# Optimization experiments

Measured on AMD Instinct MI355X. Metric: run time of the kernel, lower is better.

The kernel has to match this reference:

```python
import jax, jax.numpy as jnp
import numpy as np
from jax import lax

KSIZE = 3
SIGMA = 0.3 * ((KSIZE - 1) * 0.5 - 1) + 0.8  # cv2 auto-sigma for k=3 -> 0.8

def _gauss_kernel(k, sigma):
    ax = np.arange(k, dtype=np.float64) - (k - 1) / 2
    xx, yy = np.meshgrid(ax, ax, indexing='ij')
    ker = np.exp(-(xx ** 2 + yy ** 2) / (2.0 * sigma ** 2))
    ker /= ker.sum()
    return jnp.asarray(ker, jnp.float32)

SCHARR_X = jnp.array([[-3., 0., 3.], [-10., 0., 10.], [-3., 0., 3.]], jnp.float32)
SCHARR_Y = SCHARR_X.T  # cv2.Scharr(dy=1)

def _conv2d_reflect(img, ker):
    # img: [B,1,H,W]; cross-correlation (like cv2.filter2D) with BORDER_REFLECT_101
    p = ker.shape[0] // 2
    img = jnp.pad(img, ((0, 0), (0, 0), (p, p), (p, p)), mode='reflect')
    return lax.conv_general_dilated(img, ker[None, None], (1, 1), 'VALID')

def setup_inputs() -> dict:
    key = jax.random.key(0)
    x = jax.random.uniform(key, (8, 3, 1024, 1024), dtype=jnp.float32) * 255.0
    return {"x": x}

def reference(x):
    B, C, H, W = x.shape
    # cv2 RGB2GRAY weights
    rgb_w = jnp.array([0.299, 0.587, 0.114], dtype=x.dtype)
    gray = jnp.einsum('bchw,c->bhw', x, rgb_w)[:, None]  # [B,1,H,W]
    blurred = _conv2d_reflect(gray, _gauss_kernel(KSIZE, SIGMA))
    sx = _conv2d_reflect(blurred, SCHARR_X)
    sy = _conv2d_reflect(blurred, SCHARR_Y)
    mag = jnp.sqrt(sx * sx + sy * sy)  # L2_gradient=True
    # forward returns gradient magnitude replicated across channels
    return jnp.broadcast_to(mag, (B, C, H, W))
```

## Files before the change

### kernel.cpp

```cpp
#include <hip/hip_runtime.h>
#include <math.h>


#define IMG_H 1024
#define IMG_W 1024
#define TH 16
#define TW 128
#define GY (TH + 4)
#define GX (TW + 4)
#define BYR (TH + 2)
#define BXC (TW + 2)

#define GW0 0.52201125f
#define GW1 0.23899437f

__global__ __launch_bounds__(256)
void edge_kernel(const float* __restrict__ in, float* __restrict__ out, int B) {
    __shared__ float sg[GY][GX];
    __shared__ float sb[BYR][BXC];

    const int tid = threadIdx.x;
    const int x0 = blockIdx.x * TW;
    const int y0 = blockIdx.y * TH;
    const int b  = blockIdx.z;

    const size_t plane = (size_t)IMG_H * IMG_W;
    const float* pr = in + (size_t)b * 3 * plane;
    const float* pg = pr + plane;
    const float* pb = pg + plane;

    for (int i = tid; i < GY * GX; i += 256) {
        int gy = i / GX;
        int gx = i - gy * GX;
        int y = y0 - 2 + gy;
        int x = x0 - 2 + gx;
        y = (y < 0) ? -y : ((y >= IMG_H) ? (2 * IMG_H - 2 - y) : y);
        x = (x < 0) ? -x : ((x >= IMG_W) ? (2 * IMG_W - 2 - x) : x);
        int idx = y * IMG_W + x;
        sg[gy][gx] = 0.299f * pr[idx] + 0.587f * pg[idx] + 0.114f * pb[idx];
    }
    __syncthreads();

    for (int i = tid; i < BYR * BXC; i += 256) {
        int by = i / BXC;
        int bx = i - by * BXC;
        float h0 = GW1 * sg[by    ][bx] + GW0 * sg[by    ][bx + 1] + GW1 * sg[by    ][bx + 2];
        float h1 = GW1 * sg[by + 1][bx] + GW0 * sg[by + 1][bx + 1] + GW1 * sg[by + 1][bx + 2];
        float h2 = GW1 * sg[by + 2][bx] + GW0 * sg[by + 2][bx + 1] + GW1 * sg[by + 2][bx + 2];
        sb[by][bx] = GW1 * h0 + GW0 * h1 + GW1 * h2;
    }
    __syncthreads();

    const int tx  = tid & (TW - 1);
    const int ty0 = tid >> 7;
    float* po = out + (size_t)b * 3 * plane;
    for (int ty = ty0; ty < TH; ty += 2) {
        float a00 = sb[ty    ][tx], a01 = sb[ty    ][tx + 1], a02 = sb[ty    ][tx + 2];
        float a10 = sb[ty + 1][tx],                           a12 = sb[ty + 1][tx + 2];
        float a20 = sb[ty + 2][tx], a21 = sb[ty + 2][tx + 1], a22 = sb[ty + 2][tx + 2];
        float sx = 3.0f * (a02 - a00) + 10.0f * (a12 - a10) + 3.0f * (a22 - a20);
        float sy = 3.0f * (a20 - a00) + 10.0f * (a21 - a01) + 3.0f * (a22 - a02);
        float mag = sqrtf(sx * sx + sy * sy);
        size_t o = (size_t)(y0 + ty) * IMG_W + (x0 + tx);
        po[o]             = mag;
        po[o + plane]     = mag;
        po[o + 2 * plane] = mag;
    }
}

extern "C" void kernel_launch(void* const* d_in, const int* in_sizes, int n_in,
                              void* d_out, int out_size, void* d_ws, size_t ws_size,
                              hipStream_t stream) {
    const float* in = (const float*)d_in[0];
    float* out = (float*)d_out;
    const int B = in_sizes[0] / (3 * IMG_H * IMG_W);
    dim3 grid(IMG_W / TW, IMG_H / TH, B);
    edge_kernel<<<grid, dim3(256), 0, stream>>>(in, out, B);
}
```

Baseline: 185.5 us.

## Replace shared-memory tiles with register-resident separable 5x5 combined filter per wavefront

Folds the Gaussian blur and Scharr operators into separable 5-tap row filters (smooth and derivative) and applies them to gray values held in registers. A ring buffer keeps five rows per thread, neighbour columns come from wavefront shuffles, and only a small per-row halo is loaded. All loads and stores are now float4, and shared memory and block barriers are removed. In exchange the per-thread register count goes up, and the edge handling is more intricate because reflection and clamping have to be emulated at tile borders.

```diff
diff --git a/kernel.cpp b/kernel.cpp
--- a/kernel.cpp
+++ b/kernel.cpp
@@ -4,67 +4,104 @@
 
 #define IMG_H 1024
 #define IMG_W 1024
-#define TH 16
-#define TW 128
-#define GY (TH + 4)
-#define GX (TW + 4)
-#define BYR (TH + 2)
-#define BXC (TW + 2)
+#define SH 16
+#define SW 256
 
-#define GW0 0.52201125f
-#define GW1 0.23899437f
+#define W0 0.52201125f
+#define W1 0.23899437f
+#define AV0 0.71698311f
+#define AV1 3.95597745f
+#define AV2 6.65407872f
+
+__device__ __forceinline__ float4 gray4(float4 r, float4 g, float4 b) {
+    float4 o;
+    o.x = 0.299f * r.x + 0.587f * g.x + 0.114f * b.x;
+    o.y = 0.299f * r.y + 0.587f * g.y + 0.114f * b.y;
+    o.z = 0.299f * r.z + 0.587f * g.z + 0.114f * b.z;
+    o.w = 0.299f * r.w + 0.587f * g.w + 0.114f * b.w;
+    return o;
+}
 
 __global__ __launch_bounds__(256)
 void edge_kernel(const float* __restrict__ in, float* __restrict__ out, int B) {
-    __shared__ float sg[GY][GX];
-    __shared__ float sb[BYR][BXC];
+    const int tid  = threadIdx.x;
+    const int lane = tid & 63;
+    const int gw   = blockIdx.x * 4 + (tid >> 6);
 
-    const int tid = threadIdx.x;
-    const int x0 = blockIdx.x * TW;
-    const int y0 = blockIdx.y * TH;
-    const int b  = blockIdx.z;
+    const int ys = gw & 63;
+    const int xs = (gw >> 6) & 3;
+    const int b  = gw >> 8;
+
+    const int x0 = xs * SW;
+    const int y0 = ys * SH;
+    const int cb = x0 + 4 * lane;
 
     const size_t plane = (size_t)IMG_H * IMG_W;
     const float* pr = in + (size_t)b * 3 * plane;
     const float* pg = pr + plane;
     const float* pb = pg + plane;
+    float* po = out + (size_t)b * 3 * plane;
 
-    for (int i = tid; i < GY * GX; i += 256) {
-        int gy = i / GX;
-        int gx = i - gy * GX;
-        int y = y0 - 2 + gy;
-        int x = x0 - 2 + gx;
-        y = (y < 0) ? -y : ((y >= IMG_H) ? (2 * IMG_H - 2 - y) : y);
-        x = (x < 0) ? -x : ((x >= IMG_W) ? (2 * IMG_W - 2 - x) : x);
-        int idx = y * IMG_W + x;
-        sg[gy][gx] = 0.299f * pr[idx] + 0.587f * pg[idx] + 0.114f * pb[idx];
-    }
-    __syncthreads();
+    int hx = (lane == 0) ? (x0 - 4) : (x0 + SW);
+    hx = min(max(hx, 0), IMG_W - 4);
 
-    for (int i = tid; i < BYR * BXC; i += 256) {
-        int by = i / BXC;
-        int bx = i - by * BXC;
-        float h0 = GW1 * sg[by    ][bx] + GW0 * sg[by    ][bx + 1] + GW1 * sg[by    ][bx + 2];
-        float h1 = GW1 * sg[by + 1][bx] + GW0 * sg[by + 1][bx + 1] + GW1 * sg[by + 1][bx + 2];
-        float h2 = GW1 * sg[by + 2][bx] + GW0 * sg[by + 2][bx + 1] + GW1 * sg[by + 2][bx + 2];
-        sb[by][bx] = GW1 * h0 + GW0 * h1 + GW1 * h2;
-    }
-    __syncthreads();
+    float hs[5][4], hd[5][4];
 
-    const int tx  = tid & (TW - 1);
-    const int ty0 = tid >> 7;
-    float* po = out + (size_t)b * 3 * plane;
-    for (int ty = ty0; ty < TH; ty += 2) {
-        float a00 = sb[ty    ][tx], a01 = sb[ty    ][tx + 1], a02 = sb[ty    ][tx + 2];
-        float a10 = sb[ty + 1][tx],                           a12 = sb[ty + 1][tx + 2];
-        float a20 = sb[ty + 2][tx], a21 = sb[ty + 2][tx + 1], a22 = sb[ty + 2][tx + 2];
-        float sx = 3.0f * (a02 - a00) + 10.0f * (a12 - a10) + 3.0f * (a22 - a20);
-        float sy = 3.0f * (a20 - a00) + 10.0f * (a21 - a01) + 3.0f * (a22 - a02);
-        float mag = sqrtf(sx * sx + sy * sy);
-        size_t o = (size_t)(y0 + ty) * IMG_W + (x0 + tx);
-        po[o]             = mag;
-        po[o + plane]     = mag;
-        po[o + 2 * plane] = mag;
+    #pragma unroll
+    for (int t = 0; t < SH + 4; ++t) {
+        int yy = y0 - 2 + t;
+        yy = (yy < 0) ? -yy : ((yy >= IMG_H) ? (2 * IMG_H - 2 - yy) : yy);
+        const size_t ro = (size_t)yy << 10;
+
+        float4 r4 = *(const float4*)(pr + ro + cb);
+        float4 g4 = *(const float4*)(pg + ro + cb);
+        float4 b4 = *(const float4*)(pb + ro + cb);
+        float4 hr = *(const float4*)(pr + ro + hx);
+        float4 hg = *(const float4*)(pg + ro + hx);
+        float4 hb = *(const float4*)(pb + ro + hx);
+
+        float4 g   = gray4(r4, g4, b4);
+        float4 hgr = gray4(hr, hg, hb);
+
+        float lm2 = __shfl_up(g.z, 1);
+        float lm1 = __shfl_up(g.w, 1);
+        float rp1 = __shfl_down(g.x, 1);
+        float rp2 = __shfl_down(g.y, 1);
+        float rbx = __shfl(hgr.x, 1);
+        float rby = __shfl(hgr.y, 1);
+
+        lm2 = (lane == 0)  ? ((xs == 0) ? g.z : hgr.z) : lm2;
+        lm1 = (lane == 0)  ? ((xs == 0) ? g.y : hgr.w) : lm1;
+        rp1 = (lane == 63) ? ((xs == 3) ? g.z : rbx)   : rp1;
+        rp2 = (lane == 63) ? ((xs == 3) ? g.y : rby)   : rp2;
+
+        const float G[8] = {lm2, lm1, g.x, g.y, g.z, g.w, rp1, rp2};
+        const int ri = t % 5;
+        #pragma unroll
+        for (int k = 0; k < 4; ++k) {
+            hs[ri][k] = AV0 * (G[k] + G[k+4]) + AV1 * (G[k+1] + G[k+3]) + AV2 * G[k+2];
+            hd[ri][k] = W1 * (G[k+4] - G[k]) + W0 * (G[k+3] - G[k+1]);
+        }
+
+        if (t >= 4) {
+            const int i0 = (t+1) % 5, i1 = (t+2) % 5, i2 = (t+3) % 5,
+                      i3 = (t+4) % 5, i4 = t % 5;
+            float4 mag;
+            float* mp = &mag.x;
+            #pragma unroll
+            for (int k = 0; k < 4; ++k) {
+                float sx = AV0 * (hd[i0][k] + hd[i4][k])
+                         + AV1 * (hd[i1][k] + hd[i3][k])
+                         + AV2 * hd[i2][k];
+                float sy = W1 * (hs[i4][k] - hs[i0][k])
+                         + W0 * (hs[i3][k] - hs[i1][k]);
+                mp[k] = sqrtf(sx * sx + sy * sy);
+            }
+            size_t o = ((size_t)(y0 + t - 4) << 10) + cb;
+            *(float4*)(po + o)             = mag;
+            *(float4*)(po + o + plane)     = mag;
+            *(float4*)(po + o + 2 * plane) = mag;
+        }
     }
 }
 
@@ -74,6 +111,6 @@
     const float* in = (const float*)d_in[0];
     float* out = (float*)d_out;
     const int B = in_sizes[0] / (3 * IMG_H * IMG_W);
-    dim3 grid(IMG_W / TW, IMG_H / TH, B);
-    edge_kernel<<<grid, dim3(256), 0, stream>>>(in, out, B);
+    const int nblocks = (4 * 64 * B) / 4;
+    edge_kernel<<<dim3(nblocks), dim3(256), 0, stream>>>(in, out, B);
 }
```

Result: no change. 184.9 us (-0.3%).
